# Kernel tuning notes

Hardware: AMD Instinct MI355X
Metric: run time of the kernel (lower is better)

Reference implementation:

```python
import jax, jax.numpy as jnp
import numpy as np


def _ln(z, g, b):
    m = z.mean(-1, keepdims=True)
    v = ((z - m) ** 2).mean(-1, keepdims=True)
    return (z - m) * jax.lax.rsqrt(v + 1e-5) * g + b


def _pe(T, D):
    # standard sinusoidal positional encoding (T, D)
    pos = np.arange(T)[:, None]
    i = np.arange(D // 2)[None, :]
    ang = pos / np.power(10000.0, 2.0 * i / D)
    pe = np.zeros((T, D), dtype=np.float32)
    pe[:, 0::2] = np.sin(ang)
    pe[:, 1::2] = np.cos(ang)
    return jnp.asarray(pe)


def _whconv(z, Hinc, filt, W, b):
    # Wavelet hypergraph convolution: psi diag(filt) psi^{-1} Z W + b
    # psi = heat-kernel wavelet of normalized hypergraph Laplacian, 2nd-order Taylor (K=2, s=1)
    S = Hinc.shape[0]
    Dv = Hinc.sum(1) + 1e-6          # node degrees
    De = Hinc.sum(0) + 1e-6          # hyperedge degrees
    Hn = Hinc * (Dv ** -0.5)[:, None]
    A = (Hn / De[None, :]) @ Hn.T    # Dv^-1/2 H De^-1 H^T Dv^-1/2
    I = jnp.eye(S, dtype=z.dtype)
    L = I - A
    L2 = 0.5 * (L @ L)
    psi = I - L + L2                  # exp(-L) approx
    psi_inv = I + L + L2              # exp(+L) approx
    return psi @ (filt[:, None] * (psi_inv @ z)) @ W + b


def setup_inputs():
    S, T, F, D, NS, E, K = 2048, 64, 16, 256, 4, 128, 32
    key = jax.random.key(0)
    ks = iter(jax.random.split(key, 64))
    nrm = lambda shp: jax.random.normal(next(ks), shp, jnp.float32) * 0.02
    return dict(
        x=jax.random.normal(next(ks), (S, T, F), jnp.float32),
        snapshot=(jax.random.uniform(next(ks), (NS, S, E)) < 0.05).astype(jnp.float32),
        params_snapshot=jax.random.uniform(next(ks), (NS,), jnp.float32, 0.0, 0.99),
        beta=jnp.array([0.33, 0.33, 0.33], jnp.float32),
        W_emb=nrm((F, D)), b_emb=jnp.zeros((D,), jnp.float32),
        Wq=nrm((D, D)), bq=jnp.zeros((D,), jnp.float32),
        Wk=nrm((D, D)), bk=jnp.zeros((D,), jnp.float32),
        Wv=nrm((D, D)), bv=jnp.zeros((D,), jnp.float32),
        Wo=nrm((D, D)), bo=jnp.zeros((D,), jnp.float32),
        ln1_g=jnp.ones((D,), jnp.float32), ln1_b=jnp.zeros((D,), jnp.float32),
        W_int=nrm((D, D)), b_int=jnp.zeros((D,), jnp.float32),
        W_mix=nrm((2 * D, D)), b_mix=jnp.zeros((D,), jnp.float32),
        ln2_g=jnp.ones((D,), jnp.float32), ln2_b=jnp.zeros((D,), jnp.float32),
        Wt=nrm((D, D)), bt=jnp.zeros((D,), jnp.float32), vt=nrm((D,)),
        Wh1=nrm((D, D)), bh1=jnp.zeros((D,), jnp.float32), filt1=jnp.ones((S,), jnp.float32),
        Wh2=nrm((D, D)), bh2=jnp.zeros((D,), jnp.float32), filt2=jnp.ones((S,), jnp.float32),
        Wa=nrm((D, D)), Wb=nrm((D, D)), Wg=nrm((D, D)), bg=jnp.zeros((D,), jnp.float32),
        Wm1=nrm((D, D)), bm1=jnp.zeros((D,), jnp.float32),
        Wm2=nrm((D, 1)), bm2=jnp.zeros((1,), jnp.float32),
        num_edges=K,
    )


def reference(x, snapshot, params_snapshot, beta, W_emb, b_emb, Wq, bq, Wk, bk, Wv, bv,
              Wo, bo, ln1_g, ln1_b, W_int, b_int, W_mix, b_mix, ln2_g, ln2_b,
              Wt, bt, vt, Wh1, bh1, filt1, Wh2, bh2, filt2, Wa, Wb, Wg, bg,
              Wm1, bm1, Wm2, bm2, num_edges):
    S, T, _ = x.shape
    D = W_emb.shape[1]
    H = 8
    dh = D // H
    # feature embedding + positional encoding
    h = x @ W_emb + b_emb + _pe(T, D)
    # intra-stock (per-stock temporal) multi-head self-attention + residual + LN
    q = (h @ Wq + bq).reshape(S, T, H, dh)
    k = (h @ Wk + bk).reshape(S, T, H, dh)
    v = (h @ Wv + bv).reshape(S, T, H, dh)
    att = jax.nn.softmax(jnp.einsum('sqhd,skhd->shqk', q, k) / jnp.sqrt(jnp.float32(dh)), axis=-1)
    o = jnp.einsum('shqk,skhd->sqhd', att, v).reshape(S, T, D) @ Wo + bo
    h = _ln(h + o, ln1_g, ln1_b)
    # intensity function + mixing layer (Linear -> ReLU -> LayerNorm)
    intensity = jax.nn.softplus(h @ W_int + b_int)
    z = jax.nn.relu(jnp.concatenate([h, intensity], axis=-1) @ W_mix + b_mix)
    h = _ln(z, ln2_g, ln2_b)
    # temporal attention pooling: (S,T,D) -> (S,D)
    u = jnp.tanh(h @ Wt + bt)
    a = jax.nn.softmax(u @ vt, axis=-1)          # (S,T)
    xs = jnp.einsum('st,std->sd', a, h)           # (S,D)
    # per-snapshot two-layer wavelet hypergraph conv (dropout = eval identity)
    def per_snap(Hinc):
        r1 = jax.nn.leaky_relu(_whconv(xs, Hinc, filt1, Wh1, bh1), 0.1)
        return _whconv(r1, Hinc, filt2, Wh2, bh2)
    reps = jax.vmap(per_snap)(snapshot)           # (NS,S,D)
    hyper = jnp.einsum('n,nsd->sd', params_snapshot, reps)
    # dynamic graph learning: top-k learned similarity graph
    sim = (xs @ Wa) @ (xs @ Wb).T / jnp.sqrt(jnp.float32(D))
    kth = jax.lax.top_k(sim, num_edges)[0][:, -1]
    Adyn = jax.nn.softmax(jnp.where(sim >= kth[:, None], sim, -jnp.inf), axis=-1)
    dyn = jax.nn.relu(Adyn @ xs @ Wg + bg)
    # fusion ('sum' mode) + MLP head
    w = jax.nn.softmax(beta)
    fused = w[0] * xs + w[1] * dyn + w[2] * hyper
    return jax.nn.relu(fused @ Wm1 + bm1) @ Wm2 + bm2   # (S,1)
```

## Files before the change

### kernel.cpp

```cpp
#include <hip/hip_runtime.h>
#include <math.h>

#define S_ 2048
#define T_ 64
#define F_ 16
#define D_ 256
#define NS_ 4
#define E_ 128
#define H_ 8
#define KC_ 32
#define SD_ (S_*D_)
#define PS 264

#define PK_ATT 0
#define PK_WO  393216
#define PK_WI  524288
#define PK_WT  655360
#define PK_WM  786432
#define PKBASE 11674112

typedef __attribute__((ext_vector_type(8))) short bf16x8;
typedef __attribute__((ext_vector_type(4))) float f32x4;

__device__ __forceinline__ float warp_sum64(float v){
  #pragma unroll
  for (int o=32;o>=1;o>>=1) v += __shfl_xor(v,o);
  return v;
}
__device__ __forceinline__ float warp_max64(float v){
  #pragma unroll
  for (int o=32;o>=1;o>>=1) v = fmaxf(v,__shfl_xor(v,o));
  return v;
}
__device__ __forceinline__ float softplus_f(float v){
  return fmaxf(v,0.f) + log1pf(__expf(-fabsf(v)));
}
__device__ __forceinline__ float tanh_f(float v){
  float t = __expf(-2.f*fabsf(v));
  float r = (1.f-t)/(1.f+t);
  return copysignf(r, v);
}
__device__ __forceinline__ void splitf(float f, short& h, short& l){
  unsigned u = __float_as_uint(f);
  unsigned hb = (u + 0x7FFFu + ((u>>16)&1u)) >> 16;
  float fl = f - __uint_as_float(hb<<16);
  unsigned v = __float_as_uint(fl);
  unsigned lb = (v + 0x7FFFu + ((v>>16)&1u)) >> 16;
  h = (short)hb; l = (short)lb;
}
__device__ __forceinline__ f32x4 mfma3(bf16x8 ah, bf16x8 al, bf16x8 bh, bf16x8 bl, f32x4 c){
  c = __builtin_amdgcn_mfma_f32_16x16x32_bf16(al, bh, c, 0,0,0);
  c = __builtin_amdgcn_mfma_f32_16x16x32_bf16(ah, bl, c, 0,0,0);
  c = __builtin_amdgcn_mfma_f32_16x16x32_bf16(ah, bh, c, 0,0,0);
  return c;
}
__device__ __forceinline__ void afrag_f32(const float* base, int stride, int rbase, int ks, int lane, bf16x8& hi, bf16x8& lo){
  const float* p = base + (rbase + (lane&15))*stride + ks + ((lane>>4)<<3);
  #pragma unroll
  for (int jj=0;jj<8;++jj){ short h,l; splitf(p[jj],h,l); hi[jj]=h; lo[jj]=l; }
}
__device__ __forceinline__ bf16x8 afrag_pk(const short* plane, int rbase, int ks, int lane){
  return *(const bf16x8*)(plane + (rbase + (lane&15))*PS + ks + ((lane>>4)<<3));
}
__device__ __forceinline__ void bfrag_pk(const unsigned* pk, int tile, int lane, bf16x8& hi, bf16x8& lo){
  const unsigned* p = pk + (((tile<<6) + lane)<<3);
  #pragma unroll
  for (int jj=0;jj<8;++jj){ unsigned u=p[jj]; hi[jj]=(short)(u & 0xffffu); lo[jj]=(short)(u>>16); }
}
__device__ __forceinline__ void store_h(short* Hh, short* Hl, int r, int c, float f){
  short h,l; splitf(f,h,l);
  Hh[r*PS+c]=h; Hl[r*PS+c]=l;
}
__device__ __forceinline__ float load_h(const short* Hh, const short* Hl, int r, int c){
  int idx=r*PS+c;
  return __uint_as_float(((unsigned)(unsigned short)Hh[idx])<<16)
       + __uint_as_float(((unsigned)(unsigned short)Hl[idx])<<16);
}

__global__ void pack_qkv(const float* __restrict__ W, short* __restrict__ dst, int vplane){
  int i = blockIdx.x*256 + threadIdx.x;
  int jj=i&7, n=(i>>3)&15, q=(i>>7)&3, ntg=(i>>9)&15, kt=i>>13;
  float f = W[(kt*32 + q*8 + jj)*256 + (ntg*16+n)];
  short h,l; splitf(f,h,l);
  int hp = ntg>>2, ntl = ntg&3;
  int base = ((hp*8+kt)*6 + vplane*2)*2048;
  int local = ntl*512 + (q*16+n)*8 + jj;
  dst[base+local] = h;
  dst[base+2048+local] = l;
}
__global__ void pack_post(const float* __restrict__ W, short* __restrict__ dst){
  int i = blockIdx.x*256 + threadIdx.x;
  int jj=i&7, n=(i>>3)&15, q=(i>>7)&3, ntg=(i>>9)&15, kt=i>>13;
  float f = W[(kt*32 + q*8 + jj)*256 + (ntg*16+n)];
  short h,l; splitf(f,h,l);
  int dl = kt*16384 + ntg*512 + (q*16+n)*8 + jj;
  dst[dl] = h;
  dst[dl+8192] = l;
}

__global__ void pe_kernel(float* __restrict__ pe){
  int i = blockIdx.x*256 + threadIdx.x;
  int t = i >> 8, d = i & 255;
  int ii = d >> 1;
  float w = __expf(-(float)ii * (logf(10000.f)/128.f));
  float ang = (float)t * w;
  pe[i] = (d & 1) ? cosf(ang) : sinf(ang);
}

__launch_bounds__(512,1)
__global__ void stageA_kernel(
    const float* __restrict__ x, const float* __restrict__ pe,
    const float* __restrict__ Wemb, const float* __restrict__ bemb,
    const float* __restrict__ bq, const float* __restrict__ bk, const float* __restrict__ bv,
    const float* __restrict__ bo,
    const float* __restrict__ ln1g, const float* __restrict__ ln1b,
    const float* __restrict__ bint,
    const float* __restrict__ bmix,
    const float* __restrict__ ln2g, const float* __restrict__ ln2b,
    const float* __restrict__ bt,
    const float* __restrict__ vt,
    const short* __restrict__ pkc,
    float* __restrict__ xs)
{
  __shared__ __attribute__((aligned(16))) short hbh[64*PS];
  __shared__ __attribute__((aligned(16))) short hbl[64*PS];
  __shared__ __attribute__((aligned(16))) char smem[85504];

  short*    wst   = (short*)smem;
  unsigned* k2f2  = (unsigned*)smem;
  unsigned* v2f2  = (unsigned*)(smem + 16384);
  float*    qb2   = (float*)(smem + 32768);
  float*    scb2  = (float*)(smem + 50176);
  float*    poolb = (float*)smem;

  const int j  = threadIdx.x;
  const int s  = blockIdx.x;
  const int w  = j >> 6;
  const int lane = j & 63;
  const int m_ = lane & 15, qd = lane >> 4;
  const int rg2 = w >> 1, par = w & 1;
  const int rbase = rg2*16;
  const int rv = w*8;
  const int c0 = lane;

  {
    float* xb = (float*)smem;
    const float* xp = x + (long)s*T_*F_;
    for (int i=j; i<T_*F_; i+=512) xb[i] = xp[i];
  }
  __syncthreads();

  {
    const float* xb = (const float*)smem;
    float acc[8][4];
    #pragma unroll
    for (int r=0;r<8;++r){acc[r][0]=0;acc[r][1]=0;acc[r][2]=0;acc[r][3]=0;}
    #pragma unroll
    for (int k=0;k<F_;++k){
      float w0=Wemb[k*D_+c0], w1=Wemb[k*D_+c0+64], w2=Wemb[k*D_+c0+128], w3=Wemb[k*D_+c0+192];
      #pragma unroll
      for (int r=0;r<8;++r){
        float hv = xb[(rv+r)*F_+k];
        acc[r][0]+=hv*w0; acc[r][1]+=hv*w1; acc[r][2]+=hv*w2; acc[r][3]+=hv*w3;
      }
    }
    float b0=bemb[c0],b1=bemb[c0+64],b2=bemb[c0+128],b3=bemb[c0+192];
    __syncthreads();
    #pragma unroll
    for (int r=0;r<8;++r){
      int t = rv+r;
      store_h(hbh,hbl,t,c0,     acc[r][0]+b0+pe[t*D_+c0]);
      store_h(hbh,hbl,t,c0+64,  acc[r][1]+b1+pe[t*D_+c0+64]);
      store_h(hbh,hbl,t,c0+128, acc[r][2]+b2+pe[t*D_+c0+128]);
      store_h(hbh,hbl,t,c0+192, acc[r][3]+b3+pe[t*D_+c0+192]);
    }
  }
  __syncthreads();

  bf16x8 AH[8], AL[8];
  #pragma unroll
  for (int kt=0;kt<8;++kt){
    AH[kt] = afrag_pk(hbh, rbase, kt*32, lane);
    AL[kt] = afrag_pk(hbl, rbase, kt*32, lane);
  }

  const float rs = 0.17677669529663687f;
  f32x4 co[8];
  #pragma unroll
  for (int t=0;t<8;++t) co[t] = (f32x4){0.f,0.f,0.f,0.f};

  for (int hp=0; hp<4; ++hp){
    f32x4 qa[2],ka[2],va[2];
    #pragma unroll
    for (int t=0;t<2;++t){
      qa[t]=(f32x4){0.f,0.f,0.f,0.f};
      ka[t]=(f32x4){0.f,0.f,0.f,0.f};
      va[t]=(f32x4){0.f,0.f,0.f,0.f};
    }
    bf16x8 pre[3];
    {
      const short* b0 = pkc + PK_ATT + (hp*8)*12288;
      #pragma unroll
      for (int r=0;r<3;++r) pre[r] = *(const bf16x8*)(b0 + (j+r*512)*8);
    }
    for (int kt=0; kt<8; ++kt){
      __syncthreads();
      #pragma unroll
      for (int r=0;r<3;++r) *(bf16x8*)(wst + (j+r*512)*8) = pre[r];
      __syncthreads();
      if (kt<7){
        const short* nb = pkc + PK_ATT + (hp*8+kt+1)*12288;
        #pragma unroll
        for (int r=0;r<3;++r) pre[r] = *(const bf16x8*)(nb + (j+r*512)*8);
      }
      bf16x8 ah = AH[kt], al = AL[kt];
      #pragma unroll
      for (int t=0;t<2;++t){
        int ntl = par*2+t;
        bf16x8 bh,bl;
        bh = *(bf16x8*)(wst +         ntl*512 + lane*8);
        bl = *(bf16x8*)(wst + 2048  + ntl*512 + lane*8);
        qa[t]=mfma3(ah,al,bh,bl,qa[t]);
        bh = *(bf16x8*)(wst + 4096  + ntl*512 + lane*8);
        bl = *(bf16x8*)(wst + 6144  + ntl*512 + lane*8);
        ka[t]=mfma3(ah,al,bh,bl,ka[t]);
        bh = *(bf16x8*)(wst + 8192  + ntl*512 + lane*8);
        bl = *(bf16x8*)(wst + 10240 + ntl*512 + lane*8);
        va[t]=mfma3(ah,al,bh,bl,va[t]);
      }
    }
    __syncthreads();
    #pragma unroll
    for (int t=0;t<2;++t){
      int ntg = par*2+t;
      #pragma unroll
      for (int r=0;r<4;++r){
        int trow = rbase + qd*4 + r;
        int pcp = ntg*16 + m_;
        int head = pcp >> 5;
        int cp = pcp & 31;
        int col = hp*64 + pcp;
        qb2[trow*68 + pcp] = (qa[t][r] + bq[col]) * rs;
        short hS,lS;
        float kv2 = ka[t][r] + bk[col];
        splitf(kv2,hS,lS);
        k2f2[head*2048 + (((trow>>4)*4 + (cp>>3))*16 + (trow&15))*8 + (cp&7)]
            = (unsigned)(unsigned short)hS | ((unsigned)(unsigned short)lS<<16);
        float vv2 = va[t][r] + bv[col];
        splitf(vv2,hS,lS);
        v2f2[head*2048 + ((((trow>>5)*2 + (cp>>4))*4 + ((trow>>3)&3))*16 + (cp&15))*8 + (trow&7)]
            = (unsigned)(unsigned short)hS | ((unsigned)(unsigned short)lS<<16);
      }
    }
    __syncthreads();
    float* scb = scb2 + par*4352;
    {
      bf16x8 ah,al;
      afrag_f32(qb2, 68, rbase, par*32, lane, ah, al);
      f32x4 sc4[4];
      #pragma unroll
      for (int nt=0;nt<4;++nt){
        bf16x8 bh,bl; bfrag_pk(k2f2 + par*2048, nt, lane, bh, bl);
        sc4[nt] = mfma3(ah,al,bh,bl,(f32x4){0.f,0.f,0.f,0.f});
      }
      #pragma unroll
      for (int r=0;r<4;++r){
        float mx = fmaxf(fmaxf(sc4[0][r],sc4[1][r]),fmaxf(sc4[2][r],sc4[3][r]));
        #pragma unroll
        for (int o=8;o>=1;o>>=1) mx = fmaxf(mx, __shfl_xor(mx,o));
        float es = 0.f;
        #pragma unroll
        for (int nt=0;nt<4;++nt){ float e=__expf(sc4[nt][r]-mx); sc4[nt][r]=e; es+=e; }
        #pragma unroll
        for (int o=8;o>=1;o>>=1) es += __shfl_xor(es,o);
        float inv = 1.f/es;
        int trow = rbase + qd*4 + r;
        #pragma unroll
        for (int nt=0;nt<4;++nt) scb[trow*68 + nt*16 + m_] = sc4[nt][r]*inv;
      }
    }
    {
      f32x4 oa[2];
      oa[0]=(f32x4){0.f,0.f,0.f,0.f}; oa[1]=(f32x4){0.f,0.f,0.f,0.f};
      #pragma unroll
      for (int kt=0;kt<2;++kt){
        bf16x8 ah2,al2; afrag_f32(scb, 68, rbase, kt*32, lane, ah2, al2);
        #pragma unroll
        for (int nt=0;nt<2;++nt){
          bf16x8 bh,bl; bfrag_pk(v2f2 + par*2048, kt*2+nt, lane, bh, bl);
          oa[nt]=mfma3(ah2,al2,bh,bl,oa[nt]);
        }
      }
      #pragma unroll
      for (int nt=0;nt<2;++nt){
        #pragma unroll
        for (int r=0;r<4;++r)
          qb2[(rbase+qd*4+r)*68 + par*32 + nt*16 + m_] = oa[nt][r];
      }
    }
    __syncthreads();
    for (int ks=0; ks<2; ++ks){
      bf16x8 ah,al; afrag_f32(qb2, 68, rbase, ks*32, lane, ah, al);
      const short* wob = pkc + PK_WO + (hp*2+ks)*16384 + lane*8;
      #pragma unroll
      for (int t=0;t<8;++t){
        int ntg = 2*t+par;
        bf16x8 bh = *(const bf16x8*)(wob + ntg*512);
        bf16x8 bl = *(const bf16x8*)(wob + 8192 + ntg*512);
        co[t]=mfma3(ah,al,bh,bl,co[t]);
      }
    }
  }

  #pragma unroll
  for (int t=0;t<8;++t){
    int cc = (2*t+par)*16+m_;
    float bov = bo[cc];
    #pragma unroll
    for (int r=0;r<4;++r){
      int row = rbase+qd*4+r;
      store_h(hbh,hbl,row,cc, load_h(hbh,hbl,row,cc) + co[t][r] + bov);
    }
  }
  __syncthreads();

  {
    float g0=ln1g[c0],g1=ln1g[c0+64],g2=ln1g[c0+128],g3=ln1g[c0+192];
    float bb0=ln1b[c0],bb1=ln1b[c0+64],bb2=ln1b[c0+128],bb3=ln1b[c0+192];
    for (int rr=0;rr<8;++rr){
      int t=rv+rr;
      float v0=load_h(hbh,hbl,t,c0),    v1=load_h(hbh,hbl,t,c0+64);
      float v2=load_h(hbh,hbl,t,c0+128),v3=load_h(hbh,hbl,t,c0+192);
      float sm=warp_sum64(v0+v1+v2+v3);
      float sq=warp_sum64(v0*v0+v1*v1+v2*v2+v3*v3);
      float mean=sm*(1.f/256.f);
      float inv=rsqrtf(fmaxf(sq*(1.f/256.f)-mean*mean,0.f)+1e-5f);
      store_h(hbh,hbl,t,c0,    (v0-mean)*inv*g0+bb0);
      store_h(hbh,hbl,t,c0+64, (v1-mean)*inv*g1+bb1);
      store_h(hbh,hbl,t,c0+128,(v2-mean)*inv*g2+bb2);
      store_h(hbh,hbl,t,c0+192,(v3-mean)*inv*g3+bb3);
    }
  }
  __syncthreads();

  auto loadB=[&](bf16x8* d, const short* base, int kt){
    const short* p = base + kt*16384 + lane*8;
    d[0]=*(const bf16x8*)(p + (2*w)*512);
    d[1]=*(const bf16x8*)(p + 8192 + (2*w)*512);
    d[2]=*(const bf16x8*)(p + (2*w+1)*512);
    d[3]=*(const bf16x8*)(p + 8192 + (2*w+1)*512);
  };
  const short* BM = pkc + PK_WM;
  const short* BI = pkc + PK_WI;
  const short* BT = pkc + PK_WT;

  f32x4 az[4][2], ai[4][2];
  #pragma unroll
  for (int rt=0;rt<4;++rt){
    az[rt][0]=(f32x4){0.f,0.f,0.f,0.f}; az[rt][1]=(f32x4){0.f,0.f,0.f,0.f};
    ai[rt][0]=(f32x4){0.f,0.f,0.f,0.f}; ai[rt][1]=(f32x4){0.f,0.f,0.f,0.f};
  }
  bf16x8 cb[4], nb[4];
  loadB(cb, BM, 0);
  for (int kt=0; kt<8; ++kt){
    if (kt<7) loadB(nb, BM, kt+1); else loadB(nb, BI, 0);
    #pragma unroll
    for (int rt=0;rt<4;++rt){
      bf16x8 ah = afrag_pk(hbh, rt*16, kt*32, lane);
      bf16x8 al = afrag_pk(hbl, rt*16, kt*32, lane);
      az[rt][0]=mfma3(ah,al,cb[0],cb[1],az[rt][0]);
      az[rt][1]=mfma3(ah,al,cb[2],cb[3],az[rt][1]);
    }
    #pragma unroll
    for (int r=0;r<4;++r) cb[r]=nb[r];
  }
  for (int kt=0; kt<8; ++kt){
    if (kt<7) loadB(nb, BI, kt+1); else loadB(nb, BM, 8);
    #pragma unroll
    for (int rt=0;rt<4;++rt){
      bf16x8 ah = afrag_pk(hbh, rt*16, kt*32, lane);
      bf16x8 al = afrag_pk(hbl, rt*16, kt*32, lane);
      ai[rt][0]=mfma3(ah,al,cb[0],cb[1],ai[rt][0]);
      ai[rt][1]=mfma3(ah,al,cb[2],cb[3],ai[rt][1]);
    }
    #pragma unroll
    for (int r=0;r<4;++r) cb[r]=nb[r];
  }
  __syncthreads();
  #pragma unroll
  for (int rt=0;rt<4;++rt){
    #pragma unroll
    for (int t=0;t<2;++t){
      int col=(2*w+t)*16+m_;
      float bb=bint[col];
      #pragma unroll
      for (int r=0;r<4;++r)
        store_h(hbh,hbl, rt*16+qd*4+r, col, softplus_f(ai[rt][t][r]+bb));
    }
  }
  __syncthreads();
  for (int kt=0; kt<8; ++kt){
    if (kt<7) loadB(nb, BM, kt+9); else loadB(nb, BT, 0);
    #pragma unroll
    for (int rt=0;rt<4;++rt){
      bf16x8 ah = afrag_pk(hbh, rt*16, kt*32, lane);
      bf16x8 al = afrag_pk(hbl, rt*16, kt*32, lane);
      az[rt][0]=mfma3(ah,al,cb[0],cb[1],az[rt][0]);
      az[rt][1]=mfma3(ah,al,cb[2],cb[3],az[rt][1]);
    }
    #pragma unroll
    for (int r=0;r<4;++r) cb[r]=nb[r];
  }
  __syncthreads();
  #pragma unroll
  for (int rt=0;rt<4;++rt){
    #pragma unroll
    for (int t=0;t<2;++t){
      int col=(2*w+t)*16+m_;
      float bb=bmix[col];
      #pragma unroll
      for (int r=0;r<4;++r)
        store_h(hbh,hbl, rt*16+qd*4+r, col, fmaxf(az[rt][t][r]+bb,0.f));
    }
  }
  __syncthreads();
  {
    float g0=ln2g[c0],g1=ln2g[c0+64],g2=ln2g[c0+128],g3=ln2g[c0+192];
    float bb0=ln2b[c0],bb1=ln2b[c0+64],bb2=ln2b[c0+128],bb3=ln2b[c0+192];
    for (int rr=0;rr<8;++rr){
      int t=rv+rr;
      float v0=load_h(hbh,hbl,t,c0),    v1=load_h(hbh,hbl,t,c0+64);
      float v2=load_h(hbh,hbl,t,c0+128),v3=load_h(hbh,hbl,t,c0+192);
      float sm=warp_sum64(v0+v1+v2+v3);
      float sq=warp_sum64(v0*v0+v1*v1+v2*v2+v3*v3);
      float mean=sm*(1.f/256.f);
      float inv=rsqrtf(fmaxf(sq*(1.f/256.f)-mean*mean,0.f)+1e-5f);
      store_h(hbh,hbl,t,c0,    (v0-mean)*inv*g0+bb0);
      store_h(hbh,hbl,t,c0+64, (v1-mean)*inv*g1+bb1);
      store_h(hbh,hbl,t,c0+128,(v2-mean)*inv*g2+bb2);
      store_h(hbh,hbl,t,c0+192,(v3-mean)*inv*g3+bb3);
    }
  }
  __syncthreads();
  {
    f32x4 at4[4][2];
    #pragma unroll
    for (int rt=0;rt<4;++rt){
      at4[rt][0]=(f32x4){0.f,0.f,0.f,0.f}; at4[rt][1]=(f32x4){0.f,0.f,0.f,0.f};
    }
    for (int kt=0; kt<8; ++kt){
      if (kt<7) loadB(nb, BT, kt+1);
      #pragma unroll
      for (int rt=0;rt<4;++rt){
        bf16x8 ah = afrag_pk(hbh, rt*16, kt*32, lane);
        bf16x8 al = afrag_pk(hbl, rt*16, kt*32, lane);
        at4[rt][0]=mfma3(ah,al,cb[0],cb[1],at4[rt][0]);
        at4[rt][1]=mfma3(ah,al,cb[2],cb[3],at4[rt][1]);
      }
      #pragma unroll
      for (int r=0;r<4;++r) cb[r]=nb[r];
    }
    #pragma unroll
    for (int rt=0;rt<4;++rt){
      #pragma unroll
      for (int r=0;r<4;++r){
        int row = rt*16+qd*4+r;
        float p = 0.f;
        #pragma unroll
        for (int t=0;t<2;++t){
          int col=(2*w+t)*16+m_;
          p += tanh_f(at4[rt][t][r]+bt[col])*vt[col];
        }
        p += __shfl_xor(p,1); p += __shfl_xor(p,2);
        p += __shfl_xor(p,4); p += __shfl_xor(p,8);
        if (m_==0) poolb[w*64+row] = p;
      }
    }
  }
  __syncthreads();
  if (j < 64){
    float v = 0.f;
    #pragma unroll
    for (int ww=0;ww<8;++ww) v += poolb[ww*64+j];
    float m = warp_max64(v);
    float e = __expf(v-m);
    float ssum = warp_sum64(e);
    poolb[512+j] = e/ssum;
  }
  __syncthreads();
  if (j < 256){
    float acc=0.f;
    #pragma unroll 8
    for (int t=0;t<T_;++t) acc += poolb[512+t]*load_h(hbh,hbl,t,j);
    xs[(long)s*D_+j] = acc;
  }
}

__global__ void hg_deg(const float* __restrict__ Hinc, float* __restrict__ Dv, float* __restrict__ De){
  const int n = blockIdx.y, s0 = blockIdx.x*64;
  const float* Hp = Hinc + (long)n*S_*E_;
  const int j = threadIdx.x;
  {
    int r = j>>2, q = j&3;
    const float* rp = Hp + (long)(s0+r)*E_ + q*32;
    float sm=0;
    #pragma unroll
    for (int e=0;e<32;++e) sm += rp[e];
    sm += __shfl_xor(sm,1); sm += __shfl_xor(sm,2);
    if (q==0) Dv[n*S_+s0+r]=sm+1e-6f;
  }
  if (j < E_){
    float cs=0;
    for (int ss=0;ss<64;++ss) cs += Hp[(long)(s0+ss)*E_+j];
    atomicAdd(&De[n*E_+j], cs);
  }
}

__global__ void hg_scale(const float* __restrict__ Hinc, const float* __restrict__ Dv,
                         const float* __restrict__ De, float* __restrict__ Hn, float* __restrict__ HnD){
  long i = (long)blockIdx.x*256+threadIdx.x;
  int n = (int)(i >> 18);
  int rem = (int)(i & 262143);
  int srow = rem >> 7;
  int e = rem & 127;
  float h = Hinc[i];
  float hn = h * rsqrtf(Dv[n*S_+srow]);
  Hn[i] = hn;
  HnD[i] = hn / (De[n*E_+e]+1e-6f);
}

__launch_bounds__(256,1)
__global__ void hg_phase1(const float* __restrict__ Hn, const float* __restrict__ M,
                          long mz, float* __restrict__ Ppart)
{
  __shared__ float hl[64*E_];
  __shared__ float ml[64*128];
  const int kc = blockIdx.x, dh = blockIdx.y, n = blockIdx.z;
  const int j = threadIdx.x;
  const float* Hp = Hn + ((long)n*S_ + (long)kc*64)*E_;
  const float* Mp = M + (long)n*mz + (long)kc*64*D_ + dh*128;
  for (int i=j*4; i<64*E_; i+=1024) *(float4*)&hl[i] = *(const float4*)&Hp[i];
  for (int i=j*4; i<64*128; i+=1024){
    int row = i>>7, cc = i&127;
    *(float4*)&ml[i] = *(const float4*)&Mp[(long)row*D_ + cc];
  }
  __syncthreads();
  const int eg = j & 15, dg = j >> 4;
  float acc[8][8];
  #pragma unroll
  for (int e=0;e<8;++e){
    #pragma unroll
    for (int d=0;d<8;++d) acc[e][d]=0.f;
  }
  for (int ss=0; ss<64; ++ss){
    float hv[8], mv[8];
    *(float4*)&hv[0] = *(const float4*)&hl[ss*E_+eg*8];
    *(float4*)&hv[4] = *(const float4*)&hl[ss*E_+eg*8+4];
    *(float4*)&mv[0] = *(const float4*)&ml[ss*128+dg*8];
    *(float4*)&mv[4] = *(const float4*)&ml[ss*128+dg*8+4];
    #pragma unroll
    for (int e=0;e<8;++e){
      #pragma unroll
      for (int d=0;d<8;++d) acc[e][d] += hv[e]*mv[d];
    }
  }
  float* Pp = Ppart + (long)(n*KC_+kc)*E_*D_ + dh*128;
  #pragma unroll
  for (int e=0;e<8;++e){
    int erow = eg*8+e;
    #pragma unroll
    for (int d4=0;d4<8;d4+=4){
      float4 v = make_float4(acc[e][d4],acc[e][d4+1],acc[e][d4+2],acc[e][d4+3]);
      *(float4*)&Pp[(long)erow*D_ + dg*8 + d4] = v;
    }
  }
}

__global__ void hg_reduceP(const float* __restrict__ Ppart, float* __restrict__ P){
  const int n = blockIdx.y;
  int base = blockIdx.x*1024;
  for (int i = base + threadIdx.x; i < base+1024; i += 256){
    const float* pp = Ppart + (long)n*KC_*E_*D_ + i;
    float a = 0;
    #pragma unroll
    for (int kc=0;kc<KC_;++kc) a += pp[(long)kc*E_*D_];
    P[(long)n*E_*D_ + i] = a;
  }
}

__launch_bounds__(256,1)
__global__ void hg_phase2(const float* __restrict__ HnD, const float* __restrict__ P,
                          const float* __restrict__ X1, long x1z, float c1,
                          const float* __restrict__ X2, long x2z, float c2,
                          float c3, const float* __restrict__ filt, int usefilt,
                          float* __restrict__ out)
{
  __shared__ float al[E_*68];
  __shared__ float pl[E_*68];
  const int st = blockIdx.x*64, dt = blockIdx.y*64, n = blockIdx.z;
  const int j = threadIdx.x;
  {
    const int r = j >> 2, k0 = (j&3)*32;
    const float* hp = HnD + ((long)n*S_ + st + r)*E_ + k0;
    #pragma unroll
    for (int kk=0; kk<32; kk+=4){
      float4 v = *(const float4*)&hp[kk];
      al[(k0+kk+0)*68+r]=v.x;
      al[(k0+kk+1)*68+r]=v.y;
      al[(k0+kk+2)*68+r]=v.z;
      al[(k0+kk+3)*68+r]=v.w;
    }
  }
  for (int idx=j; idx<E_*16; idx+=256){
    int k = idx>>4, dsub = (idx&15)*4;
    *(float4*)&pl[k*68+dsub] = *(const float4*)&P[((long)n*E_+k)*D_ + dt + dsub];
  }
  __syncthreads();
  const int tx = j&15, ty = j>>4;
  float acc[4][4];
  #pragma unroll
  for (int i=0;i<4;++i){acc[i][0]=0;acc[i][1]=0;acc[i][2]=0;acc[i][3]=0;}
  for (int k=0;k<E_;++k){
    float4 a = *(const float4*)&al[k*68+ty*4];
    float4 b = *(const float4*)&pl[k*68+tx*4];
    acc[0][0]+=a.x*b.x; acc[0][1]+=a.x*b.y; acc[0][2]+=a.x*b.z; acc[0][3]+=a.x*b.w;
    acc[1][0]+=a.y*b.x; acc[1][1]+=a.y*b.y; acc[1][2]+=a.y*b.z; acc[1][3]+=a.y*b.w;
    acc[2][0]+=a.z*b.x; acc[2][1]+=a.z*b.y; acc[2][2]+=a.z*b.z; acc[2][3]+=a.z*b.w;
    acc[3][0]+=a.w*b.x; acc[3][1]+=a.w*b.y; acc[3][2]+=a.w*b.z; acc[3][3]+=a.w*b.w;
  }
  #pragma unroll
  for (int i=0;i<4;++i){
    int srow = st + ty*4 + i;
    float f = usefilt ? filt[srow] : 1.f;
    #pragma unroll
    for (int m=0;m<4;++m){
      int d = dt + tx*4+m;
      long li = (long)srow*D_ + d;
      float v = c3*acc[i][m];
      if (X1) v += c1*X1[x1z*n + li];
      if (X2) v += c2*X2[x2z*n + li];
      out[((long)n*S_ + srow)*D_ + d] = f*v;
    }
  }
}

__launch_bounds__(256,1)
__global__ void gemm_nn(const float* __restrict__ A, long az,
                        const float* __restrict__ B, long bz,
                        float* __restrict__ C, long cz,
                        int K, int N,
                        const float* __restrict__ bias, int act)
{
  __shared__ float al[32*68];
  __shared__ float bl[32*68];
  const int mt = blockIdx.x*64, nt = blockIdx.y*64, zz = blockIdx.z;
  const int j = threadIdx.x;
  const float* Ap = A + (long)az*zz;
  const float* Bp = B + (long)bz*zz;
  const int tx = j&15, ty = j>>4;
  float acc[4][4];
  #pragma unroll
  for (int i=0;i<4;++i){acc[i][0]=0;acc[i][1]=0;acc[i][2]=0;acc[i][3]=0;}
  for (int k0=0;k0<K;k0+=32){
    #pragma unroll
    for (int half=0; half<2; ++half){
      int idx = j + half*256;
      int r = idx>>3, kk=(idx&7)*4;
      float4 v = *(const float4*)&Ap[(long)(mt+r)*K + k0+kk];
      al[(kk+0)*68+r]=v.x; al[(kk+1)*68+r]=v.y; al[(kk+2)*68+r]=v.z; al[(kk+3)*68+r]=v.w;
    }
    #pragma unroll
    for (int half=0; half<2; ++half){
      int idx = j + half*256;
      int r = idx>>4, cc=(idx&15)*4;
      *(float4*)&bl[r*68+cc] = *(const float4*)&Bp[(long)(k0+r)*N + nt+cc];
    }
    __syncthreads();
    #pragma unroll
    for (int kk=0;kk<32;++kk){
      float4 a = *(const float4*)&al[kk*68+ty*4];
      float4 b = *(const float4*)&bl[kk*68+tx*4];
      acc[0][0]+=a.x*b.x; acc[0][1]+=a.x*b.y; acc[0][2]+=a.x*b.z; acc[0][3]+=a.x*b.w;
      acc[1][0]+=a.y*b.x; acc[1][1]+=a.y*b.y; acc[1][2]+=a.y*b.z; acc[1][3]+=a.y*b.w;
      acc[2][0]+=a.z*b.x; acc[2][1]+=a.z*b.y; acc[2][2]+=a.z*b.z; acc[2][3]+=a.z*b.w;
      acc[3][0]+=a.w*b.x; acc[3][1]+=a.w*b.y; acc[3][2]+=a.w*b.z; acc[3][3]+=a.w*b.w;
    }
    __syncthreads();
  }
  #pragma unroll
  for (int i=0;i<4;++i){
    int row = mt+ty*4+i;
    #pragma unroll
    for (int m=0;m<4;++m){
      int col = nt+tx*4+m;
      float v = acc[i][m];
      if (bias) v += bias[col];
      if (act==1) v = fmaxf(v,0.f);
      else if (act==2) v = (v>0.f)? v : 0.1f*v;
      C[(long)cz*zz + (long)row*N + col] = v;
    }
  }
}

__launch_bounds__(256,1)
__global__ void gemm_nt_scaled(const float* __restrict__ A, const float* __restrict__ B,
                               float* __restrict__ C, int K, float scale)
{
  __shared__ float al[32*68];
  __shared__ float bl[32*68];
  const int mt = blockIdx.x*64, nt = blockIdx.y*64;
  const int j = threadIdx.x;
  const int tx = j&15, ty = j>>4;
  float acc[4][4];
  #pragma unroll
  for (int i=0;i<4;++i){acc[i][0]=0;acc[i][1]=0;acc[i][2]=0;acc[i][3]=0;}
  for (int k0=0;k0<K;k0+=32){
    #pragma unroll
    for (int half=0; half<2; ++half){
      int idx = j + half*256;
      int r = idx>>3, kk=(idx&7)*4;
      float4 v = *(const float4*)&A[(long)(mt+r)*K + k0+kk];
      al[(kk+0)*68+r]=v.x; al[(kk+1)*68+r]=v.y; al[(kk+2)*68+r]=v.z; al[(kk+3)*68+r]=v.w;
    }
    #pragma unroll
    for (int half=0; half<2; ++half){
      int idx = j + half*256;
      int r = idx>>3, kk=(idx&7)*4;
      float4 v = *(const float4*)&B[(long)(nt+r)*K + k0+kk];
      bl[(kk+0)*68+r]=v.x; bl[(kk+1)*68+r]=v.y; bl[(kk+2)*68+r]=v.z; bl[(kk+3)*68+r]=v.w;
    }
    __syncthreads();
    #pragma unroll
    for (int kk=0;kk<32;++kk){
      float4 a = *(const float4*)&al[kk*68+ty*4];
      float4 b = *(const float4*)&bl[kk*68+tx*4];
      acc[0][0]+=a.x*b.x; acc[0][1]+=a.x*b.y; acc[0][2]+=a.x*b.z; acc[0][3]+=a.x*b.w;
      acc[1][0]+=a.y*b.x; acc[1][1]+=a.y*b.y; acc[1][2]+=a.y*b.z; acc[1][3]+=a.y*b.w;
      acc[2][0]+=a.z*b.x; acc[2][1]+=a.z*b.y; acc[2][2]+=a.z*b.z; acc[2][3]+=a.z*b.w;
      acc[3][0]+=a.w*b.x; acc[3][1]+=a.w*b.y; acc[3][2]+=a.w*b.z; acc[3][3]+=a.w*b.w;
    }
    __syncthreads();
  }
  #pragma unroll
  for (int i=0;i<4;++i){
    #pragma unroll
    for (int m=0;m<4;++m){
      C[(long)(mt+ty*4+i)*S_ + nt+tx*4+m] = acc[i][m]*scale;
    }
  }
}

__launch_bounds__(256,1)
__global__ void topk_gather(const float* __restrict__ sim, const float* __restrict__ xs,
                            const int* __restrict__ Kp, float* __restrict__ dynpre)
{
  __shared__ float row[S_];
  __shared__ float work[S_];
  __shared__ float wred[4]; __shared__ int ired[4];
  __shared__ float selw[256]; __shared__ int seli[256];
  __shared__ int cnt; __shared__ float sh_kth, sh_max, sh_den;
  const int s = blockIdx.x, j = threadIdx.x;
  const float* rp = sim + (long)s*S_;
  for (int i=j;i<S_;i+=256){ float v=rp[i]; row[i]=v; work[i]=v; }
  if (j==0) cnt=0;
  __syncthreads();
  const int K = Kp[0];
  for (int it=0; it<K; ++it){
    float m=-3.0e38f; int mi=0;
    for (int i=j;i<S_;i+=256){ float v=work[i]; if (v>m){m=v;mi=i;} }
    #pragma unroll
    for (int o=32;o>=1;o>>=1){
      float om=__shfl_xor(m,o); int oi=__shfl_xor(mi,o);
      if (om>m){m=om;mi=oi;}
    }
    if ((j&63)==0){ wred[j>>6]=m; ired[j>>6]=mi; }
    __syncthreads();
    if (j==0){
      float bm=wred[0]; int bi=ired[0];
      #pragma unroll
      for (int w=1;w<4;++w) if (wred[w]>bm){bm=wred[w];bi=ired[w];}
      work[bi]=-3.0e38f;
      if (it==0) sh_max=bm;
      sh_kth=bm;
    }
    __syncthreads();
  }
  const float kth=sh_kth, rmax=sh_max;
  for (int i=j;i<S_;i+=256){
    float v=row[i];
    if (v>=kth){
      int p=atomicAdd(&cnt,1);
      if (p<256){ seli[p]=i; selw[p]=__expf(v-rmax); }
    }
  }
  __syncthreads();
  int c = cnt; if (c>256) c=256;
  {
    float p = (j<c)? selw[j] : 0.f;
    p = warp_sum64(p);
    if ((j&63)==0) wred[j>>6]=p;
    __syncthreads();
    if (j==0) sh_den = wred[0]+wred[1]+wred[2]+wred[3];
    __syncthreads();
  }
  float acc=0.f;
  for (int l=0;l<c;++l) acc += selw[l]*xs[(long)seli[l]*D_ + j];
  dynpre[(long)s*D_+j] = acc / sh_den;
}

__global__ void hyperwsum_kernel(const float* __restrict__ reps, const float* __restrict__ ps,
                                 float* __restrict__ hyper)
{
  long idx = (long)blockIdx.x*256+threadIdx.x;
  hyper[idx] = ps[0]*reps[idx] + ps[1]*reps[(long)SD_+idx]
             + ps[2]*reps[2L*SD_+idx] + ps[3]*reps[3L*SD_+idx];
}

__global__ void fuse_kernel(const float* __restrict__ xs, const float* __restrict__ dyn,
                            const float* __restrict__ hyper, const float* __restrict__ beta,
                            float* __restrict__ fused)
{
  long idx = (long)blockIdx.x*256+threadIdx.x;
  float b0=beta[0],b1=beta[1],b2=beta[2];
  float mx=fmaxf(b0,fmaxf(b1,b2));
  float e0=__expf(b0-mx),e1=__expf(b1-mx),e2=__expf(b2-mx);
  float inv=1.f/(e0+e1+e2);
  fused[idx] = e0*inv*xs[idx] + e1*inv*dyn[idx] + e2*inv*hyper[idx];
}

__global__ void head_kernel(const float* __restrict__ hh1, const float* __restrict__ Wm2,
                            const float* __restrict__ bm2, float* __restrict__ out)
{
  int r = blockIdx.x*32 + (threadIdx.x>>3);
  int sub = threadIdx.x&7;
  const float* hp = hh1 + (long)r*D_;
  float acc=0.f;
  for (int c=sub;c<D_;c+=8) acc += hp[c]*Wm2[c];
  acc += __shfl_xor(acc,1); acc += __shfl_xor(acc,2); acc += __shfl_xor(acc,4);
  if (sub==0) out[r]=acc+bm2[0];
}

extern "C" void kernel_launch(void* const* d_in, const int* in_sizes, int n_in,
                              void* d_out, int out_size, void* d_ws, size_t ws_size,
                              hipStream_t stream)
{
  (void)in_sizes;(void)n_in;(void)out_size;(void)ws_size;
  const float* x        =(const float*)d_in[0];
  const float* snapshot =(const float*)d_in[1];
  const float* ps       =(const float*)d_in[2];
  const float* beta     =(const float*)d_in[3];
  const float* Wemb=(const float*)d_in[4];  const float* bemb=(const float*)d_in[5];
  const float* Wq  =(const float*)d_in[6];  const float* bq  =(const float*)d_in[7];
  const float* Wk  =(const float*)d_in[8];  const float* bk  =(const float*)d_in[9];
  const float* Wv  =(const float*)d_in[10]; const float* bv  =(const float*)d_in[11];
  const float* Wo  =(const float*)d_in[12]; const float* bo  =(const float*)d_in[13];
  const float* ln1g=(const float*)d_in[14]; const float* ln1b=(const float*)d_in[15];
  const float* Wint=(const float*)d_in[16]; const float* bint=(const float*)d_in[17];
  const float* Wmix=(const float*)d_in[18]; const float* bmix=(const float*)d_in[19];
  const float* ln2g=(const float*)d_in[20]; const float* ln2b=(const float*)d_in[21];
  const float* Wt  =(const float*)d_in[22]; const float* bt  =(const float*)d_in[23];
  const float* vt  =(const float*)d_in[24];
  const float* Wh1 =(const float*)d_in[25]; const float* bh1 =(const float*)d_in[26];
  const float* filt1=(const float*)d_in[27];
  const float* Wh2 =(const float*)d_in[28]; const float* bh2 =(const float*)d_in[29];
  const float* filt2=(const float*)d_in[30];
  const float* Wa  =(const float*)d_in[31]; const float* Wb  =(const float*)d_in[32];
  const float* Wg  =(const float*)d_in[33]; const float* bg  =(const float*)d_in[34];
  const float* Wm1 =(const float*)d_in[35]; const float* bm1 =(const float*)d_in[36];
  const float* Wm2 =(const float*)d_in[37]; const float* bm2 =(const float*)d_in[38];
  const int* numedges=(const int*)d_in[39];
  float* out=(float*)d_out;

  float* w = (float*)d_ws;
  float* Ppart = w;
  float* Hn    = w + 4194304;
  float* HnD   = Hn + 1048576;
  float* P     = HnD + 1048576;
  float* Dv    = P + 131072;
  float* De    = Dv + 8192;
  float* pe    = w;
  float* repsb = w;
  float* sim   = w;
  float* xs    = w + 6431232;
  float* hyper = xs + SD_;
  float* bufA  = hyper + SD_;
  float* bufB  = bufA + 4*SD_;
  float* p1    = bufA;
  float* q1    = bufA + SD_;
  float* dynpre= bufA + 2*SD_;
  float* dyn   = bufA + 3*SD_;
  float* fused = bufB;
  float* hh1   = bufB + SD_;
  short* pkc   = (short*)(w + PKBASE);

  hipMemsetAsync(De, 0, (size_t)NS_*E_*sizeof(float), stream);
  pe_kernel<<<64,256,0,stream>>>(pe);
  pack_qkv<<<256,256,0,stream>>>(Wq, pkc+PK_ATT, 0);
  pack_qkv<<<256,256,0,stream>>>(Wk, pkc+PK_ATT, 1);
  pack_qkv<<<256,256,0,stream>>>(Wv, pkc+PK_ATT, 2);
  pack_post<<<256,256,0,stream>>>(Wo,   pkc+PK_WO);
  pack_post<<<256,256,0,stream>>>(Wint, pkc+PK_WI);
  pack_post<<<256,256,0,stream>>>(Wt,   pkc+PK_WT);
  pack_post<<<512,256,0,stream>>>(Wmix, pkc+PK_WM);

  stageA_kernel<<<S_,512,0,stream>>>(x,pe,Wemb,bemb,bq,bk,bv,bo,
                                     ln1g,ln1b,bint,bmix,ln2g,ln2b,bt,vt,
                                     pkc,xs);
  hg_deg<<<dim3(32,NS_),256,0,stream>>>(snapshot,Dv,De);
  hg_scale<<<4096,256,0,stream>>>(snapshot,Dv,De,Hn,HnD);

  auto applyA=[&](const float* M, long mz,
                  const float* X1, long x1z, float c1,
                  const float* X2, long x2z, float c2, float c3,
                  const float* filt, int uf, float* outb){
    hg_phase1<<<dim3(KC_,2,NS_),256,0,stream>>>(Hn,M,mz,Ppart);
    hg_reduceP<<<dim3(32,NS_),256,0,stream>>>(Ppart,P);
    hg_phase2<<<dim3(32,4,NS_),256,0,stream>>>(HnD,P,X1,x1z,c1,X2,x2z,c2,c3,filt,uf,outb);
  };

  applyA(xs,0,     xs,0,1.f,    nullptr,0,0.f,  -1.f,  nullptr,0, bufA);
  applyA(bufA,SD_, xs,0,1.f,    bufA,SD_,1.5f,  -0.5f, filt1,1,   bufB);
  applyA(bufB,SD_, bufB,SD_,1.f, nullptr,0,0.f, -1.f,  nullptr,0, bufA);
  applyA(bufA,SD_, bufB,SD_,1.f, bufA,SD_,-0.5f,-0.5f, nullptr,0, bufA);
  gemm_nn<<<dim3(32,4,NS_),256,0,stream>>>(bufA,SD_, Wh1,0, bufB,SD_, 256,256, bh1, 2);

  applyA(bufB,SD_, bufB,SD_,1.f, nullptr,0,0.f, -1.f,  nullptr,0, bufA);
  applyA(bufA,SD_, bufB,SD_,1.f, bufA,SD_,1.5f, -0.5f, filt2,1,   bufB);
  applyA(bufB,SD_, bufB,SD_,1.f, nullptr,0,0.f, -1.f,  nullptr,0, bufA);
  applyA(bufA,SD_, bufB,SD_,1.f, bufA,SD_,-0.5f,-0.5f, nullptr,0, bufA);
  gemm_nn<<<dim3(32,4,NS_),256,0,stream>>>(bufA,SD_, Wh2,0, repsb,SD_, 256,256, bh2, 0);
  hyperwsum_kernel<<<2048,256,0,stream>>>(repsb,ps,hyper);

  gemm_nn<<<dim3(32,4,1),256,0,stream>>>(xs,0, Wa,0, p1,0, 256,256, nullptr, 0);
  gemm_nn<<<dim3(32,4,1),256,0,stream>>>(xs,0, Wb,0, q1,0, 256,256, nullptr, 0);
  gemm_nt_scaled<<<dim3(32,32),256,0,stream>>>(p1,q1,sim,256,0.0625f);
  topk_gather<<<S_,256,0,stream>>>(sim,xs,numedges,dynpre);
  gemm_nn<<<dim3(32,4,1),256,0,stream>>>(dynpre,0, Wg,0, dyn,0, 256,256, bg, 1);

  fuse_kernel<<<2048,256,0,stream>>>(xs,dyn,hyper,beta,fused);
  gemm_nn<<<dim3(32,4,1),256,0,stream>>>(fused,0, Wm1,0, hh1,0, 256,256, bm1, 1);
  head_kernel<<<64,256,0,stream>>>(hh1,Wm2,bm2,out);
}
```

Before: 1.485 ms.

## Merge weight packing, double-buffer QKV staging, restructure hypergraph reduction and top-k

Seven weight-packing launches become one 2D-grid kernel. The QKV weight staging in stageA now alternates between two LDS buffers, which removes one barrier per k-step. hg_phase1 now splits the node dimension into 4 chunks with 64x64 output tiles, down from 32 partial sums, and the separate reduceP kernel is dropped because hg_phase2 sums the 4 partials while loading. topk_gather keeps each row in registers instead of shared memory, raising occupancy. The risks are a larger LDS footprint in stageA and less parallelism in phase1 (128 blocks).

```diff
diff --git a/kernel.cpp b/kernel.cpp
--- a/kernel.cpp
+++ b/kernel.cpp
@@ -8,7 +8,6 @@
 #define NS_ 4
 #define E_ 128
 #define H_ 8
-#define KC_ 32
 #define SD_ (S_*D_)
 #define PS 264
 
@@ -77,25 +76,36 @@
        + __uint_as_float(((unsigned)(unsigned short)Hl[idx])<<16);
 }
 
-__global__ void pack_qkv(const float* __restrict__ W, short* __restrict__ dst, int vplane){
+__global__ void pack_all(const float* __restrict__ Wq, const float* __restrict__ Wk,
+                         const float* __restrict__ Wv, const float* __restrict__ Wo,
+                         const float* __restrict__ Wint, const float* __restrict__ Wt,
+                         const float* __restrict__ Wmix, short* __restrict__ pkc){
+  int y = blockIdx.y;
   int i = blockIdx.x*256 + threadIdx.x;
-  int jj=i&7, n=(i>>3)&15, q=(i>>7)&3, ntg=(i>>9)&15, kt=i>>13;
-  float f = W[(kt*32 + q*8 + jj)*256 + (ntg*16+n)];
-  short h,l; splitf(f,h,l);
-  int hp = ntg>>2, ntl = ntg&3;
-  int base = ((hp*8+kt)*6 + vplane*2)*2048;
-  int local = ntl*512 + (q*16+n)*8 + jj;
-  dst[base+local] = h;
-  dst[base+2048+local] = l;
-}
-__global__ void pack_post(const float* __restrict__ W, short* __restrict__ dst){
-  int i = blockIdx.x*256 + threadIdx.x;
-  int jj=i&7, n=(i>>3)&15, q=(i>>7)&3, ntg=(i>>9)&15, kt=i>>13;
-  float f = W[(kt*32 + q*8 + jj)*256 + (ntg*16+n)];
-  short h,l; splitf(f,h,l);
-  int dl = kt*16384 + ntg*512 + (q*16+n)*8 + jj;
-  dst[dl] = h;
-  dst[dl+8192] = l;
+  if (y < 3){
+    const float* W = (y==0)?Wq:((y==1)?Wk:Wv);
+    int jj=i&7, n=(i>>3)&15, q=(i>>7)&3, ntg=(i>>9)&15, kt=i>>13;
+    float f = W[(kt*32 + q*8 + jj)*256 + (ntg*16+n)];
+    short h,l; splitf(f,h,l);
+    int hp = ntg>>2, ntl = ntg&3;
+    int base = ((hp*8+kt)*6 + y*2)*2048;
+    int local = ntl*512 + (q*16+n)*8 + jj;
+    short* dst = pkc + PK_ATT;
+    dst[base+local] = h;
+    dst[base+2048+local] = l;
+  } else {
+    const float* W; short* dst; int ib = i;
+    if (y==3){W=Wo;   dst=pkc+PK_WO;}
+    else if (y==4){W=Wint; dst=pkc+PK_WI;}
+    else if (y==5){W=Wt;   dst=pkc+PK_WT;}
+    else if (y==6){W=Wmix; dst=pkc+PK_WM;}
+    else          {W=Wmix; dst=pkc+PK_WM; ib = i + 65536;}
+    int jj=ib&7, n=(ib>>3)&15, q=(ib>>7)&3, ntg=(ib>>9)&15, kt=ib>>13;
+    float f = W[(kt*32 + q*8 + jj)*256 + (ntg*16+n)];
+    short h,l; splitf(f,h,l);
+    int dl = kt*16384 + ntg*512 + (q*16+n)*8 + jj;
+    dst[dl] = h; dst[dl+8192] = l;
+  }
 }
 
 __global__ void pe_kernel(float* __restrict__ pe){
@@ -203,10 +213,11 @@
       #pragma unroll
       for (int r=0;r<3;++r) pre[r] = *(const bf16x8*)(b0 + (j+r*512)*8);
     }
+    __syncthreads();
     for (int kt=0; kt<8; ++kt){
-      __syncthreads();
-      #pragma unroll
-      for (int r=0;r<3;++r) *(bf16x8*)(wst + (j+r*512)*8) = pre[r];
+      short* wb = wst + (kt&1)*12288;
+      #pragma unroll
+      for (int r=0;r<3;++r) *(bf16x8*)(wb + (j+r*512)*8) = pre[r];
       __syncthreads();
       if (kt<7){
         const short* nb = pkc + PK_ATT + (hp*8+kt+1)*12288;
@@ -218,14 +229,14 @@
       for (int t=0;t<2;++t){
         int ntl = par*2+t;
         bf16x8 bh,bl;
-        bh = *(bf16x8*)(wst +         ntl*512 + lane*8);
-        bl = *(bf16x8*)(wst + 2048  + ntl*512 + lane*8);
+        bh = *(bf16x8*)(wb +         ntl*512 + lane*8);
+        bl = *(bf16x8*)(wb + 2048  + ntl*512 + lane*8);
         qa[t]=mfma3(ah,al,bh,bl,qa[t]);
-        bh = *(bf16x8*)(wst + 4096  + ntl*512 + lane*8);
-        bl = *(bf16x8*)(wst + 6144  + ntl*512 + lane*8);
+        bh = *(bf16x8*)(wb + 4096  + ntl*512 + lane*8);
+        bl = *(bf16x8*)(wb + 6144  + ntl*512 + lane*8);
         ka[t]=mfma3(ah,al,bh,bl,ka[t]);
-        bh = *(bf16x8*)(wst + 8192  + ntl*512 + lane*8);
-        bl = *(bf16x8*)(wst + 10240 + ntl*512 + lane*8);
+        bh = *(bf16x8*)(wb + 8192  + ntl*512 + lane*8);
+        bl = *(bf16x8*)(wb + 10240 + ntl*512 + lane*8);
         va[t]=mfma3(ah,al,bh,bl,va[t]);
       }
     }
@@ -529,67 +540,47 @@
   HnD[i] = hn / (De[n*E_+e]+1e-6f);
 }
 
-__launch_bounds__(256,1)
+__launch_bounds__(256,2)
 __global__ void hg_phase1(const float* __restrict__ Hn, const float* __restrict__ M,
                           long mz, float* __restrict__ Ppart)
 {
-  __shared__ float hl[64*E_];
-  __shared__ float ml[64*128];
-  const int kc = blockIdx.x, dh = blockIdx.y, n = blockIdx.z;
+  __shared__ float hl[64*64];
+  __shared__ float ml[64*64];
+  const int tile = blockIdx.x, kc = blockIdx.y, n = blockIdx.z;
+  const int et = tile>>2, dt2 = tile&3;
   const int j = threadIdx.x;
-  const float* Hp = Hn + ((long)n*S_ + (long)kc*64)*E_;
-  const float* Mp = M + (long)n*mz + (long)kc*64*D_ + dh*128;
-  for (int i=j*4; i<64*E_; i+=1024) *(float4*)&hl[i] = *(const float4*)&Hp[i];
-  for (int i=j*4; i<64*128; i+=1024){
-    int row = i>>7, cc = i&127;
-    *(float4*)&ml[i] = *(const float4*)&Mp[(long)row*D_ + cc];
-  }
-  __syncthreads();
-  const int eg = j & 15, dg = j >> 4;
-  float acc[8][8];
-  #pragma unroll
-  for (int e=0;e<8;++e){
-    #pragma unroll
-    for (int d=0;d<8;++d) acc[e][d]=0.f;
-  }
-  for (int ss=0; ss<64; ++ss){
-    float hv[8], mv[8];
-    *(float4*)&hv[0] = *(const float4*)&hl[ss*E_+eg*8];
-    *(float4*)&hv[4] = *(const float4*)&hl[ss*E_+eg*8+4];
-    *(float4*)&mv[0] = *(const float4*)&ml[ss*128+dg*8];
-    *(float4*)&mv[4] = *(const float4*)&ml[ss*128+dg*8+4];
-    #pragma unroll
-    for (int e=0;e<8;++e){
-      #pragma unroll
-      for (int d=0;d<8;++d) acc[e][d] += hv[e]*mv[d];
-    }
-  }
-  float* Pp = Ppart + (long)(n*KC_+kc)*E_*D_ + dh*128;
-  #pragma unroll
-  for (int e=0;e<8;++e){
-    int erow = eg*8+e;
-    #pragma unroll
-    for (int d4=0;d4<8;d4+=4){
-      float4 v = make_float4(acc[e][d4],acc[e][d4+1],acc[e][d4+2],acc[e][d4+3]);
-      *(float4*)&Pp[(long)erow*D_ + dg*8 + d4] = v;
-    }
-  }
-}
-
-__global__ void hg_reduceP(const float* __restrict__ Ppart, float* __restrict__ P){
-  const int n = blockIdx.y;
-  int base = blockIdx.x*1024;
-  for (int i = base + threadIdx.x; i < base+1024; i += 256){
-    const float* pp = Ppart + (long)n*KC_*E_*D_ + i;
-    float a = 0;
-    #pragma unroll
-    for (int kc=0;kc<KC_;++kc) a += pp[(long)kc*E_*D_];
-    P[(long)n*E_*D_ + i] = a;
+  const int tx = j&15, ty = j>>4;
+  float acc[4][4];
+  #pragma unroll
+  for (int i=0;i<4;++i){acc[i][0]=0;acc[i][1]=0;acc[i][2]=0;acc[i][3]=0;}
+  for (int sub=0; sub<8; ++sub){
+    int s0 = kc*512 + sub*64;
+    __syncthreads();
+    for (int i=j*4; i<4096; i+=1024){
+      int r = i>>6, c = i&63;
+      *(float4*)&hl[i] = *(const float4*)&Hn[((long)n*S_ + s0 + r)*E_ + et*64 + c];
+      *(float4*)&ml[i] = *(const float4*)&M[(long)n*mz + (long)(s0+r)*D_ + dt2*64 + c];
+    }
+    __syncthreads();
+    for (int k=0;k<64;++k){
+      float4 a = *(const float4*)&hl[k*64+ty*4];
+      float4 b = *(const float4*)&ml[k*64+tx*4];
+      acc[0][0]+=a.x*b.x; acc[0][1]+=a.x*b.y; acc[0][2]+=a.x*b.z; acc[0][3]+=a.x*b.w;
+      acc[1][0]+=a.y*b.x; acc[1][1]+=a.y*b.y; acc[1][2]+=a.y*b.z; acc[1][3]+=a.y*b.w;
+      acc[2][0]+=a.z*b.x; acc[2][1]+=a.z*b.y; acc[2][2]+=a.z*b.z; acc[2][3]+=a.z*b.w;
+      acc[3][0]+=a.w*b.x; acc[3][1]+=a.w*b.y; acc[3][2]+=a.w*b.z; acc[3][3]+=a.w*b.w;
+    }
+  }
+  float* Pp = Ppart + ((long)(n*4+kc)*E_ + et*64)*D_ + dt2*64;
+  #pragma unroll
+  for (int i=0;i<4;++i){
+    float4 v = make_float4(acc[i][0],acc[i][1],acc[i][2],acc[i][3]);
+    *(float4*)&Pp[(long)(ty*4+i)*D_ + tx*4] = v;
   }
 }
 
 __launch_bounds__(256,1)
-__global__ void hg_phase2(const float* __restrict__ HnD, const float* __restrict__ P,
+__global__ void hg_phase2(const float* __restrict__ HnD, const float* __restrict__ Ppart,
                           const float* __restrict__ X1, long x1z, float c1,
                           const float* __restrict__ X2, long x2z, float c2,
                           float c3, const float* __restrict__ filt, int usefilt,
@@ -611,9 +602,17 @@
       al[(k0+kk+3)*68+r]=v.w;
     }
   }
+  const long pkz = (long)E_*D_;
   for (int idx=j; idx<E_*16; idx+=256){
     int k = idx>>4, dsub = (idx&15)*4;
-    *(float4*)&pl[k*68+dsub] = *(const float4*)&P[((long)n*E_+k)*D_ + dt + dsub];
+    long base = ((long)(n*4)*E_ + k)*D_ + dt + dsub;
+    float4 a  = *(const float4*)&Ppart[base];
+    float4 b1 = *(const float4*)&Ppart[base + pkz];
+    float4 b2 = *(const float4*)&Ppart[base + 2*pkz];
+    float4 b3 = *(const float4*)&Ppart[base + 3*pkz];
+    a.x += b1.x+b2.x+b3.x; a.y += b1.y+b2.y+b3.y;
+    a.z += b1.z+b2.z+b3.z; a.w += b1.w+b2.w+b3.w;
+    *(float4*)&pl[k*68+dsub] = a;
   }
   __syncthreads();
   const int tx = j&15, ty = j>>4;
@@ -750,24 +749,27 @@
   }
 }
 
-__launch_bounds__(256,1)
+__launch_bounds__(256,4)
 __global__ void topk_gather(const float* __restrict__ sim, const float* __restrict__ xs,
                             const int* __restrict__ Kp, float* __restrict__ dynpre)
 {
-  __shared__ float row[S_];
-  __shared__ float work[S_];
   __shared__ float wred[4]; __shared__ int ired[4];
   __shared__ float selw[256]; __shared__ int seli[256];
-  __shared__ int cnt; __shared__ float sh_kth, sh_max, sh_den;
+  __shared__ int cnt; __shared__ float sh_kth, sh_max, sh_den; __shared__ int sh_bi;
   const int s = blockIdx.x, j = threadIdx.x;
   const float* rp = sim + (long)s*S_;
-  for (int i=j;i<S_;i+=256){ float v=rp[i]; row[i]=v; work[i]=v; }
+  float vo[8], v[8];
+  *(float4*)&vo[0] = *(const float4*)&rp[j*8];
+  *(float4*)&vo[4] = *(const float4*)&rp[j*8+4];
+  #pragma unroll
+  for (int r=0;r<8;++r) v[r]=vo[r];
   if (j==0) cnt=0;
-  __syncthreads();
   const int K = Kp[0];
   for (int it=0; it<K; ++it){
     float m=-3.0e38f; int mi=0;
-    for (int i=j;i<S_;i+=256){ float v=work[i]; if (v>m){m=v;mi=i;} }
+    #pragma unroll
+    for (int r=0;r<8;++r){ if (v[r]>m){m=v[r]; mi=r;} }
+    mi += j*8;
     #pragma unroll
     for (int o=32;o>=1;o>>=1){
       float om=__shfl_xor(m,o); int oi=__shfl_xor(mi,o);
@@ -779,18 +781,20 @@
       float bm=wred[0]; int bi=ired[0];
       #pragma unroll
       for (int w=1;w<4;++w) if (wred[w]>bm){bm=wred[w];bi=ired[w];}
-      work[bi]=-3.0e38f;
+      sh_kth=bm; sh_bi=bi;
       if (it==0) sh_max=bm;
-      sh_kth=bm;
-    }
-    __syncthreads();
+    }
+    __syncthreads();
+    int sel = sh_bi - j*8;
+    #pragma unroll
+    for (int r=0;r<8;++r) if (r==sel) v[r] = -3.0e38f;
   }
   const float kth=sh_kth, rmax=sh_max;
-  for (int i=j;i<S_;i+=256){
-    float v=row[i];
-    if (v>=kth){
+  #pragma unroll
+  for (int r=0;r<8;++r){
+    if (vo[r]>=kth){
       int p=atomicAdd(&cnt,1);
-      if (p<256){ seli[p]=i; selw[p]=__expf(v-rmax); }
+      if (p<256){ seli[p]=j*8+r; selw[p]=__expf(vo[r]-rmax); }
     }
   }
   __syncthreads();
@@ -875,8 +879,7 @@
   float* Ppart = w;
   float* Hn    = w + 4194304;
   float* HnD   = Hn + 1048576;
-  float* P     = HnD + 1048576;
-  float* Dv    = P + 131072;
+  float* Dv    = HnD + 1048576;
   float* De    = Dv + 8192;
   float* pe    = w;
   float* repsb = w;
@@ -895,13 +898,7 @@
 
   hipMemsetAsync(De, 0, (size_t)NS_*E_*sizeof(float), stream);
   pe_kernel<<<64,256,0,stream>>>(pe);
-  pack_qkv<<<256,256,0,stream>>>(Wq, pkc+PK_ATT, 0);
-  pack_qkv<<<256,256,0,stream>>>(Wk, pkc+PK_ATT, 1);
-  pack_qkv<<<256,256,0,stream>>>(Wv, pkc+PK_ATT, 2);
-  pack_post<<<256,256,0,stream>>>(Wo,   pkc+PK_WO);
-  pack_post<<<256,256,0,stream>>>(Wint, pkc+PK_WI);
-  pack_post<<<256,256,0,stream>>>(Wt,   pkc+PK_WT);
-  pack_post<<<512,256,0,stream>>>(Wmix, pkc+PK_WM);
+  pack_all<<<dim3(256,8),256,0,stream>>>(Wq,Wk,Wv,Wo,Wint,Wt,Wmix,pkc);
 
   stageA_kernel<<<S_,512,0,stream>>>(x,pe,Wemb,bemb,bq,bk,bv,bo,
                                      ln1g,ln1b,bint,bmix,ln2g,ln2b,bt,vt,
@@ -913,9 +910,8 @@
                   const float* X1, long x1z, float c1,
                   const float* X2, long x2z, float c2, float c3,
                   const float* filt, int uf, float* outb){
-    hg_phase1<<<dim3(KC_,2,NS_),256,0,stream>>>(Hn,M,mz,Ppart);
-    hg_reduceP<<<dim3(32,NS_),256,0,stream>>>(Ppart,P);
-    hg_phase2<<<dim3(32,4,NS_),256,0,stream>>>(HnD,P,X1,x1z,c1,X2,x2z,c2,c3,filt,uf,outb);
+    hg_phase1<<<dim3(8,4,NS_),256,0,stream>>>(Hn,M,mz,Ppart);
+    hg_phase2<<<dim3(32,4,NS_),256,0,stream>>>(HnD,Ppart,X1,x1z,c1,X2,x2z,c2,c3,filt,uf,outb);
   };
 
   applyA(xs,0,     xs,0,1.f,    nullptr,0,0.f,  -1.f,  nullptr,0, bufA);
```

Result: slower. 1.632 ms (+9.9%).
